# Kernel optimization log

Measured on AMD Instinct MI355X. Metric: run time of the kernel, lower is better.

The kernel has to match this reference:

```python
import jax, jax.numpy as jnp
import numpy as np

NUM_HEADS = 16
NUM_HIDDENS = 1024
NEG_INF = -1e6


def setup_inputs() -> dict:
    key = jax.random.key(0)
    ks = jax.random.split(key, 8)
    B, S, D = 2, 2048, NUM_HIDDENS
    scale = 1.0 / np.sqrt(D)
    return {
        "q": jax.random.normal(ks[0], (B, S, D), jnp.float32),
        "k": jax.random.normal(ks[1], (B, S, D), jnp.float32),
        "v": jax.random.normal(ks[2], (B, S, D), jnp.float32),
        # nn.Linear weights have shape (out_features, in_features)
        "Wq": jax.random.normal(ks[3], (D, D), jnp.float32) * scale,
        "Wk": jax.random.normal(ks[4], (D, D), jnp.float32) * scale,
        "Wv": jax.random.normal(ks[5], (D, D), jnp.float32) * scale,
        "Wo": jax.random.normal(ks[6], (D, D), jnp.float32) * scale,
        "valid_len": jax.random.randint(ks[7], (B,), 1, 2048 + 1, jnp.int32),
    }


def _unpack_heads(x, nh):
    # (B, S, H) -> (B*nh, S, H//nh), matching Unpack_base_head
    B, S, H = x.shape
    return x.reshape(B, S, nh, H // nh).transpose(0, 2, 1, 3).reshape(B * nh, S, H // nh)


def _merge_heads(x, nh):
    # Faithful to Merge_base_head: (B*nh, S, dh) -> (B, nh, S, dh)
    # -> permute(0,2,3,1) -> (B, S, dh, nh) -> (B, S, dh*nh)
    Bnh, S, dh = x.shape
    B = Bnh // nh
    x = x.reshape(B, nh, S, dh).transpose(0, 2, 3, 1)
    return x.reshape(B, S, dh * nh)


def reference(q, k, v, Wq, Wk, Wv, Wo, valid_len):
    nh = NUM_HEADS
    # projections (bias=False); Linear: x @ W.T
    qh = _unpack_heads(q @ Wq.T, nh)  # (B*nh, S, dh)
    kh = _unpack_heads(k @ Wk.T, nh)
    vh = _unpack_heads(v @ Wv.T, nh)
    dh = qh.shape[-1]
    scores = jnp.einsum("bqd,bkd->bqk", qh, kh) / jnp.sqrt(jnp.float32(dh))
    # repeat_interleave valid_len by num_heads along dim 0
    vl = jnp.repeat(valid_len, nh)  # (B*nh,)
    key_pos = jnp.arange(scores.shape[-1])  # (S,)
    mask = key_pos[None, None, :] < vl[:, None, None]  # (B*nh, 1, S)
    scores = jnp.where(mask, scores, NEG_INF)
    attn = jax.nn.softmax(scores, axis=-1)  # dropout=0.0 (eval) -> identity
    out = jnp.einsum("bqk,bkd->bqd", attn, vh)  # (B*nh, S, dh)
    out = _merge_heads(out, nh) @ Wo.T  # (B, S, H)
    return out, attn
```

## Files before the change

kernel.cpp:

```cpp
#include <hip/hip_runtime.h>
#include <stdint.h>

#define SB 2048
#define DB 1024
#define NHB 16
#define DHB 64

typedef __attribute__((ext_vector_type(8))) short short8;
typedef __attribute__((ext_vector_type(4))) short short4v;
typedef __attribute__((ext_vector_type(4))) float f32x4;

__device__ __forceinline__ unsigned short f2bf(float f) {
  union { float f; uint32_t u; } v; v.f = f;
  uint32_t u = v.u;
  return (unsigned short)((u + 0x7FFFu + ((u >> 16) & 1u)) >> 16);
}

__device__ __forceinline__ void gld16(const void* g, void* l) {
  __builtin_amdgcn_global_load_lds(
      (const __attribute__((address_space(1))) void*)g,
      (__attribute__((address_space(3))) void*)l, 16, 0, 0);
}

__device__ __forceinline__ int xcd_swz(int bid, int nwg) {
  return (bid & 7) * (nwg >> 3) + (bid >> 3);
}

struct ConvArgs {
  const float* s[7];
  unsigned short* d[7];
  int n[7];
};

__global__ __launch_bounds__(256) void conv_kernel(ConvArgs a) {
  const int t = blockIdx.y;
  const float* __restrict__ src = a.s[t];
  unsigned short* __restrict__ dst = a.d[t];
  const int n8 = a.n[t] >> 3;
  for (int i = blockIdx.x * 256 + threadIdx.x; i < n8; i += gridDim.x * 256) {
    const f32x4* p = (const f32x4*)src + (size_t)i * 2;
    f32x4 x = p[0], y = p[1];
    short8 o;
    o[0] = (short)f2bf(x[0]); o[1] = (short)f2bf(x[1]);
    o[2] = (short)f2bf(x[2]); o[3] = (short)f2bf(x[3]);
    o[4] = (short)f2bf(y[0]); o[5] = (short)f2bf(y[1]);
    o[6] = (short)f2bf(y[2]); o[7] = (short)f2bf(y[3]);
    *(short8*)(dst + (size_t)i * 8) = o;
  }
}

struct GemmArgs {
  const unsigned short* A[3];
  const unsigned short* B[3];
  void* O[3];
  int mode[3];
};

__global__ __launch_bounds__(256) void gemm128(GemmArgs ga) {
  __shared__ unsigned short SH[17408];
  unsigned short* Ab = SH;
  unsigned short* Bb = SH + 8192;

  const int z = blockIdx.y;
  const unsigned short* __restrict__ A = ga.A[z];
  const unsigned short* __restrict__ Bw = ga.B[z];
  const int mode = ga.mode[z];

  const int tid = threadIdx.x;
  const int w = tid >> 6, lane = tid & 63;
  const int g = lane >> 4, li = lane & 15;
  const int wm = w >> 1, wn = w & 1;
  const int l = xcd_swz(blockIdx.x, 256);
  const int m0 = (l >> 3) * 128, n0 = (l & 7) * 128;

  const int srow = lane >> 3;
  const int sg = (lane & 7) ^ srow;

  f32x4 acc[4][4];
  #pragma unroll
  for (int i = 0; i < 4; ++i)
    #pragma unroll
    for (int j = 0; j < 4; ++j)
      #pragma unroll
      for (int e = 0; e < 4; ++e) acc[i][j][e] = 0.f;

  for (int k0 = 0; k0 < DB; k0 += 64) {
    __syncthreads();
    #pragma unroll
    for (int i = 0; i < 4; ++i) {
      int c = w * 4 + i;
      gld16(A + (size_t)(m0 + c * 8 + srow) * DB + k0 + sg * 8, Ab + c * 512);
      gld16(Bw + (size_t)(n0 + c * 8 + srow) * DB + k0 + sg * 8, Bb + c * 512);
    }
    __syncthreads();
    short8 af[4][2], bf[4][2];
    #pragma unroll
    for (int mf = 0; mf < 4; ++mf)
      #pragma unroll
      for (int ks = 0; ks < 2; ++ks)
        af[mf][ks] = *(const short8*)&Ab[(wm * 64 + mf * 16 + li) * 64 +
                                         (((ks * 4 + g) ^ (li & 7)) << 3)];
    #pragma unroll
    for (int nf = 0; nf < 4; ++nf)
      #pragma unroll
      for (int ks = 0; ks < 2; ++ks)
        bf[nf][ks] = *(const short8*)&Bb[(wn * 64 + nf * 16 + li) * 64 +
                                         (((ks * 4 + g) ^ (li & 7)) << 3)];
    __builtin_amdgcn_s_setprio(1);
    #pragma unroll
    for (int ks = 0; ks < 2; ++ks)
      #pragma unroll
      for (int mf = 0; mf < 4; ++mf)
        #pragma unroll
        for (int nf = 0; nf < 4; ++nf)
          acc[mf][nf] = __builtin_amdgcn_mfma_f32_16x16x32_bf16(
              af[mf][ks], bf[nf][ks], acc[mf][nf], 0, 0, 0);
    __builtin_amdgcn_s_setprio(0);
  }

  if (mode == 0) {
    unsigned short* O = (unsigned short*)ga.O[z];
    #pragma unroll
    for (int mf = 0; mf < 4; ++mf)
      #pragma unroll
      for (int nf = 0; nf < 4; ++nf)
        #pragma unroll
        for (int r = 0; r < 4; ++r) {
          int row = m0 + wm * 64 + mf * 16 + g * 4 + r;
          int col = n0 + wn * 64 + nf * 16 + li;
          int b_ = row >> 11, s_ = row & 2047;
          int h = col >> 6, dp = col & 63;
          O[((size_t)(b_ * NHB + h) * SB + s_) * DHB + dp] = f2bf(acc[mf][nf][r]);
        }
  } else {
    unsigned short* O = (unsigned short*)ga.O[z];
    __syncthreads();
    #pragma unroll
    for (int mf = 0; mf < 4; ++mf)
      #pragma unroll
      for (int nf = 0; nf < 4; ++nf) {
        short4v pk;
        #pragma unroll
        for (int r = 0; r < 4; ++r) pk[r] = (short)f2bf(acc[mf][nf][r]);
        *(short4v*)&SH[(size_t)(wn * 64 + nf * 16 + li) * 136 +
                       wm * 64 + mf * 16 + g * 4] = pk;
      }
    __syncthreads();
    int c = tid >> 1, rh = tid & 1;
    int col = n0 + c;
    int h = col >> 6, dp = col & 63;
    int b_ = m0 >> 11, s0 = (m0 & 2047) + rh * 64;
    unsigned short* dst = O + ((size_t)(b_ * NHB + h) * DHB + dp) * SB + s0;
    #pragma unroll
    for (int j = 0; j < 8; ++j)
      *(short8*)(dst + j * 8) = *(const short8*)&SH[c * 136 + rh * 64 + j * 8];
  }
}

__global__ __launch_bounds__(256) void attn_kernel(
    const unsigned short* __restrict__ Qh, const unsigned short* __restrict__ Kh,
    const unsigned short* __restrict__ Vt, const int* __restrict__ valid_len,
    float* __restrict__ attn_out, unsigned short* __restrict__ Mg)
{
  __shared__ unsigned short Kb[2][4096];
  __shared__ unsigned short Vb[2][4096];
  __shared__ unsigned short QP[128][88];

  const int tid = threadIdx.x;
  const int wave = tid >> 6, lane = tid & 63;
  const int g = lane >> 4, li = lane & 15;
  const int lsw = xcd_swz(blockIdx.x, 512);
  const int q0 = (lsw & 15) * 128;
  const int bh = lsw >> 4;
  const int b_ = bh >> 4;
  const int vl = valid_len[b_];
  const int nkt = min(32, (vl + 63) >> 6);

  const int srow = lane >> 3;
  const int sg = (lane & 7) ^ srow;

  {
    int qr = tid >> 1, half = (tid & 1) * 32;
    const unsigned short* src = Qh + ((size_t)bh * SB + q0 + qr) * DHB + half;
    #pragma unroll
    for (int j = 0; j < 4; ++j)
      *(short8*)&QP[qr][half + j * 8] = *(const short8*)(src + j * 8);
  }
  __syncthreads();

  short8 qa[2][2];
  #pragma unroll
  for (int qf = 0; qf < 2; ++qf)
    #pragma unroll
    for (int ks = 0; ks < 2; ++ks)
      qa[qf][ks] = *(const short8*)&QP[wave * 32 + qf * 16 + li][ks * 32 + g * 8];

  float mQ[2] = {-1e30f, -1e30f}, lQ[2] = {0.f, 0.f};

  {
    #pragma unroll
    for (int i = 0; i < 2; ++i) {
      int c = wave * 2 + i;
      gld16(Kh + ((size_t)bh * SB + 0 + c * 8 + srow) * DHB + sg * 8,
            &Kb[0][c * 512]);
    }
    int cur = 0;
    for (int kti = 0; kti < nkt; ++kti) {
      const int kt = kti * 64;
      __syncthreads();
      if (kti + 1 < nkt) {
        #pragma unroll
        for (int i = 0; i < 2; ++i) {
          int c = wave * 2 + i;
          gld16(Kh + ((size_t)bh * SB + kt + 64 + c * 8 + srow) * DHB + sg * 8,
                &Kb[cur ^ 1][c * 512]);
        }
      }
      f32x4 sc[2][4];
      #pragma unroll
      for (int qf = 0; qf < 2; ++qf)
        #pragma unroll
        for (int nf = 0; nf < 4; ++nf)
          #pragma unroll
          for (int j = 0; j < 4; ++j) sc[qf][nf][j] = 0.f;
      __builtin_amdgcn_s_setprio(1);
      #pragma unroll
      for (int ks = 0; ks < 2; ++ks)
        #pragma unroll
        for (int nf = 0; nf < 4; ++nf) {
          short8 kbf = *(const short8*)&Kb[cur][(nf * 16 + li) * 64 +
                                               (((ks * 4 + g) ^ (li & 7)) << 3)];
          #pragma unroll
          for (int qf = 0; qf < 2; ++qf)
            sc[qf][nf] = __builtin_amdgcn_mfma_f32_16x16x32_bf16(
                kbf, qa[qf][ks], sc[qf][nf], 0, 0, 0);
        }
      __builtin_amdgcn_s_setprio(0);
      #pragma unroll
      for (int qf = 0; qf < 2; ++qf) {
        float tm = -1e30f;
        #pragma unroll
        for (int nf = 0; nf < 4; ++nf)
          #pragma unroll
          for (int r = 0; r < 4; ++r) {
            int key = kt + nf * 16 + g * 4 + r;
            float s = sc[qf][nf][r] * 0.125f;
            s = (key < vl) ? s : -1e6f;
            sc[qf][nf][r] = s;
            tm = fmaxf(tm, s);
          }
        float mo = mQ[qf], mn = fmaxf(mo, tm);
        float la = lQ[qf] * __expf(mo - mn);
        #pragma unroll
        for (int nf = 0; nf < 4; ++nf)
          #pragma unroll
          for (int r = 0; r < 4; ++r) la += __expf(sc[qf][nf][r] - mn);
        mQ[qf] = mn;
        lQ[qf] = la;
      }
      cur ^= 1;
    }
  }
  __syncthreads();

  float rlQ[2];
  #pragma unroll
  for (int qf = 0; qf < 2; ++qf) {
    float M = mQ[qf];
    M = fmaxf(M, __shfl_xor(M, 16));
    M = fmaxf(M, __shfl_xor(M, 32));
    float L = lQ[qf] * __expf(mQ[qf] - M);
    L += __shfl_xor(L, 16);
    L += __shfl_xor(L, 32);
    mQ[qf] = M;
    rlQ[qf] = 1.f / L;
  }

  f32x4 oacc[2][4];
  #pragma unroll
  for (int qf = 0; qf < 2; ++qf)
    #pragma unroll
    for (int nf = 0; nf < 4; ++nf)
      #pragma unroll
      for (int j = 0; j < 4; ++j) oacc[qf][nf][j] = 0.f;

  {
    #pragma unroll
    for (int i = 0; i < 2; ++i) {
      int c = wave * 2 + i;
      gld16(Kh + ((size_t)bh * SB + c * 8 + srow) * DHB + sg * 8, &Kb[0][c * 512]);
      gld16(Vt + ((size_t)bh * DHB + c * 8 + srow) * SB + 0 + sg * 8, &Vb[0][c * 512]);
    }
    int cur = 0;
    for (int kti = 0; kti < nkt; ++kti) {
      const int kt = kti * 64;
      __syncthreads();
      if (kti + 1 < nkt) {
        #pragma unroll
        for (int i = 0; i < 2; ++i) {
          int c = wave * 2 + i;
          gld16(Kh + ((size_t)bh * SB + kt + 64 + c * 8 + srow) * DHB + sg * 8,
                &Kb[cur ^ 1][c * 512]);
          gld16(Vt + ((size_t)bh * DHB + c * 8 + srow) * SB + kt + 64 + sg * 8,
                &Vb[cur ^ 1][c * 512]);
        }
      }
      f32x4 sc[2][4];
      #pragma unroll
      for (int qf = 0; qf < 2; ++qf)
        #pragma unroll
        for (int nf = 0; nf < 4; ++nf)
          #pragma unroll
          for (int j = 0; j < 4; ++j) sc[qf][nf][j] = 0.f;
      __builtin_amdgcn_s_setprio(1);
      #pragma unroll
      for (int ks = 0; ks < 2; ++ks)
        #pragma unroll
        for (int nf = 0; nf < 4; ++nf) {
          short8 kbf = *(const short8*)&Kb[cur][(nf * 16 + li) * 64 +
                                               (((ks * 4 + g) ^ (li & 7)) << 3)];
          #pragma unroll
          for (int qf = 0; qf < 2; ++qf)
            sc[qf][nf] = __builtin_amdgcn_mfma_f32_16x16x32_bf16(
                kbf, qa[qf][ks], sc[qf][nf], 0, 0, 0);
        }
      __builtin_amdgcn_s_setprio(0);
      #pragma unroll
      for (int qf = 0; qf < 2; ++qf) {
        int qrow = q0 + wave * 32 + qf * 16 + li;
        #pragma unroll
        for (int nf = 0; nf < 4; ++nf) {
          short4v pk;
          #pragma unroll
          for (int r = 0; r < 4; ++r) {
            int key = kt + nf * 16 + g * 4 + r;
            float s = sc[qf][nf][r] * 0.125f;
            s = (key < vl) ? s : -1e6f;
            float p = __expf(s - mQ[qf]) * rlQ[qf];
            sc[qf][nf][r] = p;
            pk[r] = (short)f2bf(p);
          }
          __builtin_nontemporal_store(
              sc[qf][nf],
              (f32x4*)(attn_out + (size_t)bh * SB * SB + (size_t)qrow * SB +
                       kt + nf * 16 + g * 4));
          *(short4v*)&QP[wave * 32 + qf * 16 + li][nf * 16 + g * 4] = pk;
        }
      }
      __builtin_amdgcn_s_setprio(1);
      #pragma unroll
      for (int ks = 0; ks < 2; ++ks) {
        short8 vbf[4];
        #pragma unroll
        for (int nf = 0; nf < 4; ++nf)
          vbf[nf] = *(const short8*)&Vb[cur][(nf * 16 + li) * 64 +
                                             (((ks * 4 + g) ^ (li & 7)) << 3)];
        #pragma unroll
        for (int qf = 0; qf < 2; ++qf) {
          short8 pa = *(const short8*)&QP[wave * 32 + qf * 16 + li][ks * 32 + g * 8];
          #pragma unroll
          for (int nf = 0; nf < 4; ++nf)
            oacc[qf][nf] = __builtin_amdgcn_mfma_f32_16x16x32_bf16(
                pa, vbf[nf], oacc[qf][nf], 0, 0, 0);
        }
      }
      __builtin_amdgcn_s_setprio(0);
      cur ^= 1;
    }
  }

  {
    int c0 = nkt * 64;
    int rem4 = (SB - c0) >> 2;
    if (rem4 > 0) {
      f32x4 z;
      z[0] = 0.f; z[1] = 0.f; z[2] = 0.f; z[3] = 0.f;
      for (int row = 0; row < 128; ++row) {
        float* dst = attn_out + (size_t)bh * SB * SB + (size_t)(q0 + row) * SB + c0;
        for (int c = tid; c < rem4; c += 256)
          __builtin_nontemporal_store(z, (f32x4*)dst + c);
      }
    }
  }

  const int h = bh & 15;
  #pragma unroll
  for (int qf = 0; qf < 2; ++qf)
    #pragma unroll
    for (int nf = 0; nf < 4; ++nf)
      #pragma unroll
      for (int r = 0; r < 4; ++r) {
        int qrow = q0 + wave * 32 + qf * 16 + g * 4 + r;
        int dp = nf * 16 + li;
        Mg[((size_t)b_ * SB + qrow) * DB + dp * NHB + h] = f2bf(oacc[qf][nf][r]);
      }
}

__global__ __launch_bounds__(256) void outproj_kernel(
    const unsigned short* __restrict__ A, const unsigned short* __restrict__ Bw,
    float* __restrict__ Out)
{
  __shared__ unsigned short SH[12288];
  unsigned short* Ab = SH;
  unsigned short* Bb = SH + 8192;

  const int tid = threadIdx.x;
  const int w = tid >> 6, lane = tid & 63;
  const int g = lane >> 4, li = lane & 15;
  const int wm = w >> 1, wn = w & 1;
  const int l = xcd_swz(blockIdx.x, 512);
  const int m0 = (l >> 4) * 128, n0 = (l & 15) * 64;

  const int srow = lane >> 3;
  const int sg = (lane & 7) ^ srow;

  int a_off[4][2], b_off[2][2];
  #pragma unroll
  for (int mf = 0; mf < 4; ++mf) {
    int row = wm * 64 + mf * 16 + li;
    #pragma unroll
    for (int ks = 0; ks < 2; ++ks)
      a_off[mf][ks] = row * 64 + (((ks * 4 + g) ^ (li & 7)) << 3);
  }
  #pragma unroll
  for (int nf = 0; nf < 2; ++nf) {
    int row = wn * 32 + nf * 16 + li;
    #pragma unroll
    for (int ks = 0; ks < 2; ++ks)
      b_off[nf][ks] = row * 64 + (((ks * 4 + g) ^ (li & 7)) << 3);
  }

  f32x4 acc[4][2];
  #pragma unroll
  for (int i = 0; i < 4; ++i)
    #pragma unroll
    for (int j = 0; j < 2; ++j)
      #pragma unroll
      for (int e = 0; e < 4; ++e) acc[i][j][e] = 0.f;

  for (int k0 = 0; k0 < DB; k0 += 64) {
    __syncthreads();
    #pragma unroll
    for (int i = 0; i < 4; ++i) {
      int c = w * 4 + i;
      gld16(A + (size_t)(m0 + c * 8 + srow) * DB + k0 + sg * 8, Ab + c * 512);
    }
    #pragma unroll
    for (int i = 0; i < 2; ++i) {
      int c = w * 2 + i;
      gld16(Bw + (size_t)(n0 + c * 8 + srow) * DB + k0 + sg * 8, Bb + c * 512);
    }
    __syncthreads();
    short8 af[4][2], bf[2][2];
    #pragma unroll
    for (int mf = 0; mf < 4; ++mf)
      #pragma unroll
      for (int ks = 0; ks < 2; ++ks)
        af[mf][ks] = *(const short8*)&Ab[a_off[mf][ks]];
    #pragma unroll
    for (int nf = 0; nf < 2; ++nf)
      #pragma unroll
      for (int ks = 0; ks < 2; ++ks)
        bf[nf][ks] = *(const short8*)&Bb[b_off[nf][ks]];
    __builtin_amdgcn_s_setprio(1);
    #pragma unroll
    for (int ks = 0; ks < 2; ++ks)
      #pragma unroll
      for (int mf = 0; mf < 4; ++mf)
        #pragma unroll
        for (int nf = 0; nf < 2; ++nf)
          acc[mf][nf] = __builtin_amdgcn_mfma_f32_16x16x32_bf16(
              af[mf][ks], bf[nf][ks], acc[mf][nf], 0, 0, 0);
    __builtin_amdgcn_s_setprio(0);
  }

  #pragma unroll
  for (int mf = 0; mf < 4; ++mf)
    #pragma unroll
    for (int nf = 0; nf < 2; ++nf)
      #pragma unroll
      for (int r = 0; r < 4; ++r) {
        int row = m0 + wm * 64 + mf * 16 + g * 4 + r;
        int col = n0 + wn * 32 + nf * 16 + li;
        Out[(size_t)row * DB + col] = acc[mf][nf][r];
      }
}

extern "C" void kernel_launch(void* const* d_in, const int* in_sizes, int n_in,
                              void* d_out, int out_size, void* d_ws, size_t ws_size,
                              hipStream_t stream) {
  const float* q  = (const float*)d_in[0];
  const float* k  = (const float*)d_in[1];
  const float* v  = (const float*)d_in[2];
  const float* Wq = (const float*)d_in[3];
  const float* Wk = (const float*)d_in[4];
  const float* Wv = (const float*)d_in[5];
  const float* Wo = (const float*)d_in[6];
  const int* vlen = (const int*)d_in[7];

  const size_t HS = (size_t)2 * NHB * SB * DHB;
  const size_t WS = (size_t)DB * DB;

  unsigned short* ws = (unsigned short*)d_ws;
  unsigned short* qb  = ws;
  unsigned short* kb  = qb + HS;
  unsigned short* vb  = kb + HS;
  unsigned short* Wqb = vb + HS;
  unsigned short* Wkb = Wqb + WS;
  unsigned short* Wvb = Wkb + WS;
  unsigned short* Wob = Wvb + WS;
  unsigned short* Qh  = Wob + WS;
  unsigned short* Kh  = Qh + HS;
  unsigned short* Vt  = Kh + HS;
  unsigned short* Mg  = qb;

  float* out  = (float*)d_out;
  float* attn = out + (size_t)2 * SB * DB;

  ConvArgs ca;
  ca.s[0] = q;  ca.d[0] = qb;  ca.n[0] = (int)HS;
  ca.s[1] = k;  ca.d[1] = kb;  ca.n[1] = (int)HS;
  ca.s[2] = v;  ca.d[2] = vb;  ca.n[2] = (int)HS;
  ca.s[3] = Wq; ca.d[3] = Wqb; ca.n[3] = (int)WS;
  ca.s[4] = Wk; ca.d[4] = Wkb; ca.n[4] = (int)WS;
  ca.s[5] = Wv; ca.d[5] = Wvb; ca.n[5] = (int)WS;
  ca.s[6] = Wo; ca.d[6] = Wob; ca.n[6] = (int)WS;

  GemmArgs pa;
  pa.A[0] = qb;  pa.A[1] = kb;  pa.A[2] = vb;
  pa.B[0] = Wqb; pa.B[1] = Wkb; pa.B[2] = Wvb;
  pa.O[0] = Qh;  pa.O[1] = Kh;  pa.O[2] = Vt;
  pa.mode[0] = 0; pa.mode[1] = 0; pa.mode[2] = 1;

  dim3 blk(256);
  conv_kernel<<<dim3(1024, 7), blk, 0, stream>>>(ca);
  gemm128<<<dim3(256, 3), blk, 0, stream>>>(pa);
  attn_kernel<<<dim3(512), blk, 0, stream>>>(Qh, Kh, Vt, vlen, attn, Mg);
  outproj_kernel<<<dim3(512), blk, 0, stream>>>(Mg, Wob, out);
}
```

Before: 247.2 us.

## Overlap attention zero-fill with projection GEMM and drop softmax running max

Extra workgroups appended to the QKV projection GEMM launch write zeros to the masked tail columns of the attention matrix, so these stores overlap projection compute instead of trailing the attention kernel. The first softmax pass no longer tracks a running maximum; it sums exp2 of prescaled scores directly, and the second pass normalises by that sum. This removes max reductions, shuffles and rescaling. In exchange, overflow safety now relies on the scores staying small.

```diff
diff --git a/kernel.cpp b/kernel.cpp
--- a/kernel.cpp
+++ b/kernel.cpp
@@ -9,6 +9,8 @@
 typedef __attribute__((ext_vector_type(8))) short short8;
 typedef __attribute__((ext_vector_type(4))) short short4v;
 typedef __attribute__((ext_vector_type(4))) float f32x4;
+
+#define SC2 0.18033688011112042f
 
 __device__ __forceinline__ unsigned short f2bf(float f) {
   union { float f; uint32_t u; } v; v.f = f;
@@ -56,8 +58,27 @@
   int mode[3];
 };
 
-__global__ __launch_bounds__(256) void gemm128(GemmArgs ga) {
+__global__ __launch_bounds__(256) void gemm128(GemmArgs ga, const int* __restrict__ vlen,
+                                               float* __restrict__ attn_out) {
   __shared__ unsigned short SH[17408];
+
+  if (blockIdx.x >= 256) {
+    const int NF = 258;
+    const int fid = blockIdx.y * 86 + (blockIdx.x - 256);
+    f32x4 z;
+    z[0] = 0.f; z[1] = 0.f; z[2] = 0.f; z[3] = 0.f;
+    const int vls[2] = {vlen[0], vlen[1]};
+    for (int rw = fid; rw < 32 * SB; rw += NF) {
+      int bh = rw >> 11, row = rw & 2047;
+      int vl = vls[bh >> 4];
+      int c0 = min(32, (vl + 63) >> 6) * 64;
+      float* dst = attn_out + (size_t)bh * SB * SB + (size_t)row * SB;
+      for (int c4 = (c0 >> 2) + threadIdx.x; c4 < (SB >> 2); c4 += 256)
+        __builtin_nontemporal_store(z, (f32x4*)dst + c4);
+    }
+    return;
+  }
+
   unsigned short* Ab = SH;
   unsigned short* Bb = SH + 8192;
 
@@ -195,7 +216,7 @@
     for (int ks = 0; ks < 2; ++ks)
       qa[qf][ks] = *(const short8*)&QP[wave * 32 + qf * 16 + li][ks * 32 + g * 8];
 
-  float mQ[2] = {-1e30f, -1e30f}, lQ[2] = {0.f, 0.f};
+  float lQ[2] = {0.f, 0.f};
 
   {
     #pragma unroll
@@ -238,25 +259,16 @@
       __builtin_amdgcn_s_setprio(0);
       #pragma unroll
       for (int qf = 0; qf < 2; ++qf) {
-        float tm = -1e30f;
+        float la = 0.f;
         #pragma unroll
         for (int nf = 0; nf < 4; ++nf)
           #pragma unroll
           for (int r = 0; r < 4; ++r) {
             int key = kt + nf * 16 + g * 4 + r;
-            float s = sc[qf][nf][r] * 0.125f;
-            s = (key < vl) ? s : -1e6f;
-            sc[qf][nf][r] = s;
-            tm = fmaxf(tm, s);
+            float s2 = (key < vl) ? sc[qf][nf][r] * SC2 : -1.5e6f;
+            la += exp2f(s2);
           }
-        float mo = mQ[qf], mn = fmaxf(mo, tm);
-        float la = lQ[qf] * __expf(mo - mn);
-        #pragma unroll
-        for (int nf = 0; nf < 4; ++nf)
-          #pragma unroll
-          for (int r = 0; r < 4; ++r) la += __expf(sc[qf][nf][r] - mn);
-        mQ[qf] = mn;
-        lQ[qf] = la;
+        lQ[qf] += la;
       }
       cur ^= 1;
     }
@@ -266,13 +278,9 @@
   float rlQ[2];
   #pragma unroll
   for (int qf = 0; qf < 2; ++qf) {
-    float M = mQ[qf];
-    M = fmaxf(M, __shfl_xor(M, 16));
-    M = fmaxf(M, __shfl_xor(M, 32));
-    float L = lQ[qf] * __expf(mQ[qf] - M);
+    float L = lQ[qf];
     L += __shfl_xor(L, 16);
     L += __shfl_xor(L, 32);
-    mQ[qf] = M;
     rlQ[qf] = 1.f / L;
   }
 
@@ -334,9 +342,8 @@
           #pragma unroll
           for (int r = 0; r < 4; ++r) {
             int key = kt + nf * 16 + g * 4 + r;
-            float s = sc[qf][nf][r] * 0.125f;
-            s = (key < vl) ? s : -1e6f;
-            float p = __expf(s - mQ[qf]) * rlQ[qf];
+            float s2 = (key < vl) ? sc[qf][nf][r] * SC2 : -1.5e6f;
+            float p = exp2f(s2) * rlQ[qf];
             sc[qf][nf][r] = p;
             pk[r] = (short)f2bf(p);
           }
@@ -366,20 +373,6 @@
       }
       __builtin_amdgcn_s_setprio(0);
       cur ^= 1;
-    }
-  }
-
-  {
-    int c0 = nkt * 64;
-    int rem4 = (SB - c0) >> 2;
-    if (rem4 > 0) {
-      f32x4 z;
-      z[0] = 0.f; z[1] = 0.f; z[2] = 0.f; z[3] = 0.f;
-      for (int row = 0; row < 128; ++row) {
-        float* dst = attn_out + (size_t)bh * SB * SB + (size_t)(q0 + row) * SB + c0;
-        for (int c = tid; c < rem4; c += 256)
-          __builtin_nontemporal_store(z, (f32x4*)dst + c);
-      }
     }
   }
 
@@ -534,7 +527,7 @@
 
   dim3 blk(256);
   conv_kernel<<<dim3(1024, 7), blk, 0, stream>>>(ca);
-  gemm128<<<dim3(256, 3), blk, 0, stream>>>(pa);
+  gemm128<<<dim3(342, 3), blk, 0, stream>>>(pa, vlen, attn);
   attn_kernel<<<dim3(512), blk, 0, stream>>>(Qh, Kh, Vt, vlen, attn, Mg);
   outproj_kernel<<<dim3(512), blk, 0, stream>>>(Mg, Wob, out);
 }
```

New measurement: 258.4 us. +4.5%, slower.

## Halve attention query tile, drop running max and double buffering, remap blocks per XCD

Applied to the files above, without the earlier changes.

The attention kernel now uses 64-query tiles with 1024 blocks. Each wave handles 16 query rows instead of 32. K/V double buffering is replaced by single buffers loaded synchronously between two barriers, which cuts LDS use and raises occupancy. The online max tracking is removed and exp2 is applied to the raw scaled scores, assuming they cannot overflow for these input magnitudes. The block-to-(bh, q-tile) mapping is rearranged so each XCD handles particular heads for L2 locality. Risks include losing the load/compute overlap and overflow when scores are large.

```diff
diff --git a/kernel.cpp b/kernel.cpp
--- a/kernel.cpp
+++ b/kernel.cpp
@@ -9,6 +9,8 @@
 typedef __attribute__((ext_vector_type(8))) short short8;
 typedef __attribute__((ext_vector_type(4))) short short4v;
 typedef __attribute__((ext_vector_type(4))) float f32x4;
+
+#define SC2 0.18033688011112042f
 
 __device__ __forceinline__ unsigned short f2bf(float f) {
   union { float f; uint32_t u; } v; v.f = f;
@@ -162,16 +164,17 @@
     const unsigned short* __restrict__ Vt, const int* __restrict__ valid_len,
     float* __restrict__ attn_out, unsigned short* __restrict__ Mg)
 {
-  __shared__ unsigned short Kb[2][4096];
-  __shared__ unsigned short Vb[2][4096];
-  __shared__ unsigned short QP[128][88];
+  __shared__ unsigned short Kb[4096];
+  __shared__ unsigned short Vb[4096];
+  __shared__ unsigned short QP[64][88];
 
   const int tid = threadIdx.x;
   const int wave = tid >> 6, lane = tid & 63;
   const int g = lane >> 4, li = lane & 15;
-  const int lsw = xcd_swz(blockIdx.x, 512);
-  const int q0 = (lsw & 15) * 128;
-  const int bh = lsw >> 4;
+  const int lsw = xcd_swz(blockIdx.x, 1024);
+  const int xcd = lsw >> 7, j = lsw & 127;
+  const int bh = ((j >> 6) << 4) + xcd * 2 + ((j >> 5) & 1);
+  const int q0 = (j & 31) * 64;
   const int b_ = bh >> 4;
   const int vl = valid_len[b_];
   const int nkt = min(32, (vl + 63) >> 6);
@@ -180,193 +183,131 @@
   const int sg = (lane & 7) ^ srow;
 
   {
-    int qr = tid >> 1, half = (tid & 1) * 32;
-    const unsigned short* src = Qh + ((size_t)bh * SB + q0 + qr) * DHB + half;
-    #pragma unroll
-    for (int j = 0; j < 4; ++j)
-      *(short8*)&QP[qr][half + j * 8] = *(const short8*)(src + j * 8);
+    int qr = tid >> 2, cs = (tid & 3) * 16;
+    const unsigned short* src = Qh + ((size_t)bh * SB + q0 + qr) * DHB + cs;
+    *(short8*)&QP[qr][cs]     = *(const short8*)src;
+    *(short8*)&QP[qr][cs + 8] = *(const short8*)(src + 8);
   }
   __syncthreads();
 
-  short8 qa[2][2];
-  #pragma unroll
-  for (int qf = 0; qf < 2; ++qf)
-    #pragma unroll
-    for (int ks = 0; ks < 2; ++ks)
-      qa[qf][ks] = *(const short8*)&QP[wave * 32 + qf * 16 + li][ks * 32 + g * 8];
-
-  float mQ[2] = {-1e30f, -1e30f}, lQ[2] = {0.f, 0.f};
-
-  {
-    #pragma unroll
-    for (int i = 0; i < 2; ++i) {
-      int c = wave * 2 + i;
-      gld16(Kh + ((size_t)bh * SB + 0 + c * 8 + srow) * DHB + sg * 8,
-            &Kb[0][c * 512]);
-    }
-    int cur = 0;
-    for (int kti = 0; kti < nkt; ++kti) {
-      const int kt = kti * 64;
-      __syncthreads();
-      if (kti + 1 < nkt) {
+  short8 qa[2];
+  #pragma unroll
+  for (int ks = 0; ks < 2; ++ks)
+    qa[ks] = *(const short8*)&QP[wave * 16 + li][ks * 32 + g * 8];
+
+  float lQ = 0.f;
+
+  for (int kti = 0; kti < nkt; ++kti) {
+    const int kt = kti * 64;
+    __syncthreads();
+    {
+      int c = wave * 2;
+      gld16(Kh + ((size_t)bh * SB + kt + c * 8 + srow) * DHB + sg * 8,
+            &Kb[c * 512]);
+      gld16(Kh + ((size_t)bh * SB + kt + (c + 1) * 8 + srow) * DHB + sg * 8,
+            &Kb[(c + 1) * 512]);
+    }
+    __syncthreads();
+    f32x4 sc[4];
+    #pragma unroll
+    for (int nf = 0; nf < 4; ++nf)
+      #pragma unroll
+      for (int e = 0; e < 4; ++e) sc[nf][e] = 0.f;
+    __builtin_amdgcn_s_setprio(1);
+    #pragma unroll
+    for (int ks = 0; ks < 2; ++ks)
+      #pragma unroll
+      for (int nf = 0; nf < 4; ++nf) {
+        short8 kbf = *(const short8*)&Kb[(nf * 16 + li) * 64 +
+                                         (((ks * 4 + g) ^ (li & 7)) << 3)];
+        sc[nf] = __builtin_amdgcn_mfma_f32_16x16x32_bf16(kbf, qa[ks], sc[nf], 0, 0, 0);
+      }
+    __builtin_amdgcn_s_setprio(0);
+    float la = 0.f;
+    #pragma unroll
+    for (int nf = 0; nf < 4; ++nf)
+      #pragma unroll
+      for (int r = 0; r < 4; ++r) {
+        int key = kt + nf * 16 + g * 4 + r;
+        float s2 = (key < vl) ? sc[nf][r] * SC2 : -1.5e6f;
+        la += exp2f(s2);
+      }
+    lQ += la;
+  }
+
+  float L = lQ;
+  L += __shfl_xor(L, 16);
+  L += __shfl_xor(L, 32);
+  const float rlQ = 1.f / L;
+
+  f32x4 oacc[4];
+  #pragma unroll
+  for (int nf = 0; nf < 4; ++nf)
+    #pragma unroll
+    for (int e = 0; e < 4; ++e) oacc[nf][e] = 0.f;
+
+  for (int kti = 0; kti < nkt; ++kti) {
+    const int kt = kti * 64;
+    __syncthreads();
+    {
+      int c = wave * 2;
+      gld16(Kh + ((size_t)bh * SB + kt + c * 8 + srow) * DHB + sg * 8,
+            &Kb[c * 512]);
+      gld16(Kh + ((size_t)bh * SB + kt + (c + 1) * 8 + srow) * DHB + sg * 8,
+            &Kb[(c + 1) * 512]);
+      gld16(Vt + ((size_t)bh * DHB + c * 8 + srow) * SB + kt + sg * 8,
+            &Vb[c * 512]);
+      gld16(Vt + ((size_t)bh * DHB + (c + 1) * 8 + srow) * SB + kt + sg * 8,
+            &Vb[(c + 1) * 512]);
+    }
+    __syncthreads();
+    f32x4 sc[4];
+    #pragma unroll
+    for (int nf = 0; nf < 4; ++nf)
+      #pragma unroll
+      for (int e = 0; e < 4; ++e) sc[nf][e] = 0.f;
+    __builtin_amdgcn_s_setprio(1);
+    #pragma unroll
+    for (int ks = 0; ks < 2; ++ks)
+      #pragma unroll
+      for (int nf = 0; nf < 4; ++nf) {
+        short8 kbf = *(const short8*)&Kb[(nf * 16 + li) * 64 +
+                                         (((ks * 4 + g) ^ (li & 7)) << 3)];
+        sc[nf] = __builtin_amdgcn_mfma_f32_16x16x32_bf16(kbf, qa[ks], sc[nf], 0, 0, 0);
+      }
+    __builtin_amdgcn_s_setprio(0);
+    {
+      int qrow = q0 + wave * 16 + li;
+      #pragma unroll
+      for (int nf = 0; nf < 4; ++nf) {
+        short4v pk;
         #pragma unroll
-        for (int i = 0; i < 2; ++i) {
-          int c = wave * 2 + i;
-          gld16(Kh + ((size_t)bh * SB + kt + 64 + c * 8 + srow) * DHB + sg * 8,
-                &Kb[cur ^ 1][c * 512]);
+        for (int r = 0; r < 4; ++r) {
+          int key = kt + nf * 16 + g * 4 + r;
+          float s2 = (key < vl) ? sc[nf][r] * SC2 : -1.5e6f;
+          float p = exp2f(s2) * rlQ;
+          sc[nf][r] = p;
+          pk[r] = (short)f2bf(p);
         }
-      }
-      f32x4 sc[2][4];
-      #pragma unroll
-      for (int qf = 0; qf < 2; ++qf)
-        #pragma unroll
-        for (int nf = 0; nf < 4; ++nf)
-          #pragma unroll
-          for (int j = 0; j < 4; ++j) sc[qf][nf][j] = 0.f;
-      __builtin_amdgcn_s_setprio(1);
-      #pragma unroll
-      for (int ks = 0; ks < 2; ++ks)
-        #pragma unroll
-        for (int nf = 0; nf < 4; ++nf) {
-          short8 kbf = *(const short8*)&Kb[cur][(nf * 16 + li) * 64 +
-                                               (((ks * 4 + g) ^ (li & 7)) << 3)];
-          #pragma unroll
-          for (int qf = 0; qf < 2; ++qf)
-            sc[qf][nf] = __builtin_amdgcn_mfma_f32_16x16x32_bf16(
-                kbf, qa[qf][ks], sc[qf][nf], 0, 0, 0);
-        }
-      __builtin_amdgcn_s_setprio(0);
-      #pragma unroll
-      for (int qf = 0; qf < 2; ++qf) {
-        float tm = -1e30f;
-        #pragma unroll
-        for (int nf = 0; nf < 4; ++nf)
-          #pragma unroll
-          for (int r = 0; r < 4; ++r) {
-            int key = kt + nf * 16 + g * 4 + r;
-            float s = sc[qf][nf][r] * 0.125f;
-            s = (key < vl) ? s : -1e6f;
-            sc[qf][nf][r] = s;
-            tm = fmaxf(tm, s);
-          }
-        float mo = mQ[qf], mn = fmaxf(mo, tm);
-        float la = lQ[qf] * __expf(mo - mn);
-        #pragma unroll
-        for (int nf = 0; nf < 4; ++nf)
-          #pragma unroll
-          for (int r = 0; r < 4; ++r) la += __expf(sc[qf][nf][r] - mn);
-        mQ[qf] = mn;
-        lQ[qf] = la;
-      }
-      cur ^= 1;
-    }
-  }
-  __syncthreads();
-
-  float rlQ[2];
-  #pragma unroll
-  for (int qf = 0; qf < 2; ++qf) {
-    float M = mQ[qf];
-    M = fmaxf(M, __shfl_xor(M, 16));
-    M = fmaxf(M, __shfl_xor(M, 32));
-    float L = lQ[qf] * __expf(mQ[qf] - M);
-    L += __shfl_xor(L, 16);
-    L += __shfl_xor(L, 32);
-    mQ[qf] = M;
-    rlQ[qf] = 1.f / L;
-  }
-
-  f32x4 oacc[2][4];
-  #pragma unroll
-  for (int qf = 0; qf < 2; ++qf)
-    #pragma unroll
-    for (int nf = 0; nf < 4; ++nf)
-      #pragma unroll
-      for (int j = 0; j < 4; ++j) oacc[qf][nf][j] = 0.f;
-
-  {
-    #pragma unroll
-    for (int i = 0; i < 2; ++i) {
-      int c = wave * 2 + i;
-      gld16(Kh + ((size_t)bh * SB + c * 8 + srow) * DHB + sg * 8, &Kb[0][c * 512]);
-      gld16(Vt + ((size_t)bh * DHB + c * 8 + srow) * SB + 0 + sg * 8, &Vb[0][c * 512]);
-    }
-    int cur = 0;
-    for (int kti = 0; kti < nkt; ++kti) {
-      const int kt = kti * 64;
-      __syncthreads();
-      if (kti + 1 < nkt) {
-        #pragma unroll
-        for (int i = 0; i < 2; ++i) {
-          int c = wave * 2 + i;
-          gld16(Kh + ((size_t)bh * SB + kt + 64 + c * 8 + srow) * DHB + sg * 8,
-                &Kb[cur ^ 1][c * 512]);
-          gld16(Vt + ((size_t)bh * DHB + c * 8 + srow) * SB + kt + 64 + sg * 8,
-                &Vb[cur ^ 1][c * 512]);
-        }
-      }
-      f32x4 sc[2][4];
-      #pragma unroll
-      for (int qf = 0; qf < 2; ++qf)
-        #pragma unroll
-        for (int nf = 0; nf < 4; ++nf)
-          #pragma unroll
-          for (int j = 0; j < 4; ++j) sc[qf][nf][j] = 0.f;
-      __builtin_amdgcn_s_setprio(1);
-      #pragma unroll
-      for (int ks = 0; ks < 2; ++ks)
-        #pragma unroll
-        for (int nf = 0; nf < 4; ++nf) {
-          short8 kbf = *(const short8*)&Kb[cur][(nf * 16 + li) * 64 +
-                                               (((ks * 4 + g) ^ (li & 7)) << 3)];
-          #pragma unroll
-          for (int qf = 0; qf < 2; ++qf)
-            sc[qf][nf] = __builtin_amdgcn_mfma_f32_16x16x32_bf16(
-                kbf, qa[qf][ks], sc[qf][nf], 0, 0, 0);
-        }
-      __builtin_amdgcn_s_setprio(0);
-      #pragma unroll
-      for (int qf = 0; qf < 2; ++qf) {
-        int qrow = q0 + wave * 32 + qf * 16 + li;
-        #pragma unroll
-        for (int nf = 0; nf < 4; ++nf) {
-          short4v pk;
-          #pragma unroll
-          for (int r = 0; r < 4; ++r) {
-            int key = kt + nf * 16 + g * 4 + r;
-            float s = sc[qf][nf][r] * 0.125f;
-            s = (key < vl) ? s : -1e6f;
-            float p = __expf(s - mQ[qf]) * rlQ[qf];
-            sc[qf][nf][r] = p;
-            pk[r] = (short)f2bf(p);
-          }
-          __builtin_nontemporal_store(
-              sc[qf][nf],
-              (f32x4*)(attn_out + (size_t)bh * SB * SB + (size_t)qrow * SB +
-                       kt + nf * 16 + g * 4));
-          *(short4v*)&QP[wave * 32 + qf * 16 + li][nf * 16 + g * 4] = pk;
-        }
-      }
-      __builtin_amdgcn_s_setprio(1);
-      #pragma unroll
-      for (int ks = 0; ks < 2; ++ks) {
-        short8 vbf[4];
-        #pragma unroll
-        for (int nf = 0; nf < 4; ++nf)
-          vbf[nf] = *(const short8*)&Vb[cur][(nf * 16 + li) * 64 +
-                                             (((ks * 4 + g) ^ (li & 7)) << 3)];
-        #pragma unroll
-        for (int qf = 0; qf < 2; ++qf) {
-          short8 pa = *(const short8*)&QP[wave * 32 + qf * 16 + li][ks * 32 + g * 8];
-          #pragma unroll
-          for (int nf = 0; nf < 4; ++nf)
-            oacc[qf][nf] = __builtin_amdgcn_mfma_f32_16x16x32_bf16(
-                pa, vbf[nf], oacc[qf][nf], 0, 0, 0);
-        }
-      }
-      __builtin_amdgcn_s_setprio(0);
-      cur ^= 1;
-    }
+        __builtin_nontemporal_store(
+            sc[nf],
+            (f32x4*)(attn_out + (size_t)bh * SB * SB + (size_t)qrow * SB +
+                     kt + nf * 16 + g * 4));
+        *(short4v*)&QP[wave * 16 + li][nf * 16 + g * 4] = pk;
+      }
+    }
+    __builtin_amdgcn_s_setprio(1);
+    #pragma unroll
+    for (int ks = 0; ks < 2; ++ks) {
+      short8 pa = *(const short8*)&QP[wave * 16 + li][ks * 32 + g * 8];
+      #pragma unroll
+      for (int nf = 0; nf < 4; ++nf) {
+        short8 vbf = *(const short8*)&Vb[(nf * 16 + li) * 64 +
+                                         (((ks * 4 + g) ^ (li & 7)) << 3)];
+        oacc[nf] = __builtin_amdgcn_mfma_f32_16x16x32_bf16(pa, vbf, oacc[nf], 0, 0, 0);
+      }
+    }
+    __builtin_amdgcn_s_setprio(0);
   }
 
   {
@@ -375,7 +316,7 @@
     if (rem4 > 0) {
       f32x4 z;
       z[0] = 0.f; z[1] = 0.f; z[2] = 0.f; z[3] = 0.f;
-      for (int row = 0; row < 128; ++row) {
+      for (int row = 0; row < 64; ++row) {
         float* dst = attn_out + (size_t)bh * SB * SB + (size_t)(q0 + row) * SB + c0;
         for (int c = tid; c < rem4; c += 256)
           __builtin_nontemporal_store(z, (f32x4*)dst + c);
@@ -385,15 +326,13 @@
 
   const int h = bh & 15;
   #pragma unroll
-  for (int qf = 0; qf < 2; ++qf)
-    #pragma unroll
-    for (int nf = 0; nf < 4; ++nf)
-      #pragma unroll
-      for (int r = 0; r < 4; ++r) {
-        int qrow = q0 + wave * 32 + qf * 16 + g * 4 + r;
-        int dp = nf * 16 + li;
-        Mg[((size_t)b_ * SB + qrow) * DB + dp * NHB + h] = f2bf(oacc[qf][nf][r]);
-      }
+  for (int nf = 0; nf < 4; ++nf)
+    #pragma unroll
+    for (int r = 0; r < 4; ++r) {
+      int qrow = q0 + wave * 16 + g * 4 + r;
+      int dp = nf * 16 + li;
+      Mg[((size_t)b_ * SB + qrow) * DB + dp * NHB + h] = f2bf(oacc[nf][r]);
+    }
 }
 
 __global__ __launch_bounds__(256) void outproj_kernel(
@@ -535,6 +474,6 @@
   dim3 blk(256);
   conv_kernel<<<dim3(1024, 7), blk, 0, stream>>>(ca);
   gemm128<<<dim3(256, 3), blk, 0, stream>>>(pa);
-  attn_kernel<<<dim3(512), blk, 0, stream>>>(Qh, Kh, Vt, vlen, attn, Mg);
+  attn_kernel<<<dim3(1024), blk, 0, stream>>>(Qh, Kh, Vt, vlen, attn, Mg);
   outproj_kernel<<<dim3(512), blk, 0, stream>>>(Mg, Wob, out);
 }
```

Result: faster. 235.7 us (-4.6%).
